# Kernel tuning notes

Measured on AMD Instinct MI355X. Metric: run time of the kernel, lower is better.

Reference implementation:

```python
import jax, jax.numpy as jnp
import numpy as np

N, E, H, NF, EF = 50000, 400000, 128, 10, 10


def setup_inputs() -> dict:
    key = jax.random.key(0)
    ks = iter(jax.random.split(key, 24))
    rn = lambda shape, s=0.1: jax.random.normal(next(ks), shape, jnp.float32) * s
    z = lambda shape: jnp.zeros(shape, jnp.float32)
    o = lambda shape: jnp.ones(shape, jnp.float32)
    return {
        "x": jax.random.normal(next(ks), (N, NF), jnp.float32),
        "edge_index": jax.random.randint(next(ks), (2, E), 0, N, jnp.int32),
        "edge_attr": jax.random.normal(next(ks), (E, EF), jnp.float32),
        "ne_w": rn((NF, H)), "ne_b": z(H), "ne_g": o(H), "ne_beta": z(H),
        "ee_w": rn((EF, H)), "ee_b": z(H), "ee_g": o(H), "ee_beta": z(H),
        "gate_w": rn((3 * H, H)), "gate_b": z(H),
        "gatA_w": rn((2, H, H)), "gatA_asrc": rn((2, 8, 16)), "gatA_adst": rn((2, 8, 16)), "gatA_bias": z((2, H)),
        "gatB_w": rn((H, H)), "gatB_asrc": rn((1, H)), "gatB_adst": rn((1, H)), "gatB_bias": z(H),
        "ln_g": o((3, H)), "ln_b": z((3, H)),
        "c1_w": rn((2 * H, H)), "c1_b": z(H), "cl1_g": o(H), "cl1_b": z(H),
        "c2_w": rn((H, H // 2)), "c2_b": z(H // 2), "cl2_g": o(H // 2), "cl2_b": z(H // 2),
        "c3_w": rn((H // 2, 2)), "c3_b": z(2),
    }


def _ln(x, g, b):
    m = x.mean(-1, keepdims=True)
    v = ((x - m) ** 2).mean(-1, keepdims=True)
    return (x - m) / jnp.sqrt(v + 1e-5) * g + b


def _gat(h, src, dst, n, w, asrc, adst, bias, concat):
    # PyG GATConv: lin (no bias), per-edge leaky_relu score, segment softmax over dst, scatter-add
    heads, dout = asrc.shape
    xp = (h @ w).reshape(n, heads, dout)             # [N, heads, dout]
    a_s = (xp * asrc).sum(-1)                        # [N, heads]
    a_d = (xp * adst).sum(-1)
    e = jax.nn.leaky_relu(a_s[src] + a_d[dst], 0.2)  # [E2, heads]
    m = jax.ops.segment_max(e, dst, num_segments=n)
    ex = jnp.exp(e - m[dst])
    s = jax.ops.segment_sum(ex, dst, num_segments=n)
    alpha = ex / s[dst]                               # [E2, heads]
    out = jax.ops.segment_sum(xp[src] * alpha[..., None], dst, num_segments=n)  # [N, heads, dout]
    out = out.reshape(n, heads * dout) if concat else out.mean(1)
    return out + bias


def reference(x, edge_index, edge_attr, ne_w, ne_b, ne_g, ne_beta, ee_w, ee_b, ee_g, ee_beta,
              gate_w, gate_b, gatA_w, gatA_asrc, gatA_adst, gatA_bias, gatB_w, gatB_asrc,
              gatB_adst, gatB_bias, ln_g, ln_b, c1_w, c1_b, cl1_g, cl1_b, c2_w, c2_b,
              cl2_g, cl2_b, c3_w, c3_b):
    n = x.shape[0]
    row, col = edge_index[0], edge_index[1]
    loops = jnp.arange(n, dtype=edge_index.dtype)     # GATConv add_self_loops=True
    src_sl = jnp.concatenate([row, loops])
    dst_sl = jnp.concatenate([col, loops])

    h = jax.nn.relu(_ln(x @ ne_w + ne_b, ne_g, ne_beta))      # node encoder (dropout=eval)
    for l in range(2):
        h = _gat(h, src_sl, dst_sl, n, gatA_w[l], gatA_asrc[l], gatA_adst[l], gatA_bias[l], True)
        h = jax.nn.relu(_ln(h, ln_g[l], ln_b[l]))
    h = _gat(h, src_sl, dst_sl, n, gatB_w, gatB_asrc, gatB_adst, gatB_bias, False)
    h = jax.nn.relu(_ln(h, ln_g[2], ln_b[2]))

    s = h[row]
    d = h[col]
    e = jax.nn.relu(_ln(edge_attr @ ee_w + ee_b, ee_g, ee_beta))  # edge encoder
    gate = jax.nn.sigmoid(jnp.concatenate([s, d, e], axis=1) @ gate_w + gate_b)
    s = s + gate * e
    d = d + gate * e

    zc = jax.nn.relu(_ln(jnp.concatenate([s, d], axis=1) @ c1_w + c1_b, cl1_g, cl1_b))
    zc = jax.nn.relu(_ln(zc @ c2_w + c2_b, cl2_g, cl2_b))
    return zc @ c3_w + c3_b                                   # [E, num_classes]
```

## Files before the change

### kernel.cpp

```cpp
#include <hip/hip_runtime.h>
#include <hip/hip_bf16.h>

#define H 128
#define NFEAT 10
#define EFEAT 10
#define XPS 144

typedef __attribute__((ext_vector_type(8))) short bf16x8;
typedef __attribute__((ext_vector_type(4))) float f32x4;
typedef __attribute__((ext_vector_type(16))) float f32x16;
typedef __attribute__((ext_vector_type(4))) unsigned u32x4;
typedef __attribute__((ext_vector_type(2))) unsigned u32x2;

__device__ __forceinline__ float bflo(unsigned v) { return __uint_as_float(v << 16); }
__device__ __forceinline__ float bfhi(unsigned v) { return __uint_as_float(v & 0xffff0000u); }
__device__ __forceinline__ unsigned bfpack(float a, float b) {
    __hip_bfloat16 h0 = __float2bfloat16(a), h1 = __float2bfloat16(b);
    return (unsigned)(*(unsigned short*)&h0) | ((unsigned)(*(unsigned short*)&h1) << 16);
}
__device__ __forceinline__ bf16x8 cast8(u32x4 v) { return __builtin_bit_cast(bf16x8, v); }

__device__ __forceinline__ bf16x8 frag_from_pack(const unsigned* w, int b2) {
    u32x4 t;
    t.x = w[b2 * 4 + 0];
    t.y = w[b2 * 4 + 1];
    t.z = w[b2 * 4 + 2];
    t.w = w[b2 * 4 + 3];
    return cast8(t);
}

__device__ __forceinline__ void ld8(bf16x8* dst, const __hip_bfloat16* base, int slot0, int l) {
#pragma unroll
    for (int i = 0; i < 8; i++)
        dst[i] = *(const bf16x8*)(base + ((size_t)(slot0 + i) * 64 + l) * 8);
}
__device__ __forceinline__ void ld4(bf16x8* dst, const __hip_bfloat16* base, int slot0, int l) {
#pragma unroll
    for (int i = 0; i < 4; i++)
        dst[i] = *(const bf16x8*)(base + ((size_t)(slot0 + i) * 64 + l) * 8);
}
__device__ __forceinline__ void mma8(f32x16* acc, const bf16x8* wb, bf16x8 bb0, bf16x8 bb1) {
#pragma unroll
    for (int mt = 0; mt < 4; mt++)
        acc[mt] = __builtin_amdgcn_mfma_f32_32x32x16_bf16(wb[mt], bb0, acc[mt], 0, 0, 0);
#pragma unroll
    for (int mt = 0; mt < 4; mt++)
        acc[mt] = __builtin_amdgcn_mfma_f32_32x32x16_bf16(wb[4 + mt], bb1, acc[mt], 0, 0, 0);
}
__device__ __forceinline__ void mma4x2(f32x16* acc, const bf16x8* wb, bf16x8 bb0, bf16x8 bb1) {
#pragma unroll
    for (int mt = 0; mt < 2; mt++)
        acc[mt] = __builtin_amdgcn_mfma_f32_32x32x16_bf16(wb[mt], bb0, acc[mt], 0, 0, 0);
#pragma unroll
    for (int mt = 0; mt < 2; mt++)
        acc[mt] = __builtin_amdgcn_mfma_f32_32x32x16_bf16(wb[2 + mt], bb1, acc[mt], 0, 0, 0);
}

template<int NT>
__device__ __forceinline__ void bias_ln_relu_pack(f32x16* acc, const float* __restrict__ bias,
        const float* __restrict__ g, const float* __restrict__ beta,
        int hh, float invn, unsigned (*pk)[8]) {
    float sm = 0.f;
#pragma unroll
    for (int m = 0; m < NT; m++) {
#pragma unroll
        for (int P = 0; P < 4; P++) {
            f32x4 bv = *(const f32x4*)&bias[m * 32 + P * 8 + hh * 4];
#pragma unroll
            for (int u = 0; u < 4; u++) {
                float v = acc[m][P * 4 + u] + bv[u];
                acc[m][P * 4 + u] = v;
                sm += v;
            }
        }
    }
    sm += __shfl_xor(sm, 32, 64);
    float mean = sm * invn;
    float q = 0.f;
#pragma unroll
    for (int m = 0; m < NT; m++) {
#pragma unroll
        for (int r = 0; r < 16; r++) { float d = acc[m][r] - mean; q += d * d; }
    }
    q += __shfl_xor(q, 32, 64);
    float rstd = rsqrtf(q * invn + 1e-5f);
#pragma unroll
    for (int m = 0; m < NT; m++) {
#pragma unroll
        for (int P = 0; P < 4; P++) {
            f32x4 gv = *(const f32x4*)&g[m * 32 + P * 8 + hh * 4];
            f32x4 bz = *(const f32x4*)&beta[m * 32 + P * 8 + hh * 4];
#pragma unroll
            for (int u = 0; u < 4; u++) {
                float y = fmaxf((acc[m][P * 4 + u] - mean) * rstd * gv[u] + bz[u], 0.f);
                acc[m][P * 4 + u] = y;
            }
        }
    }
#pragma unroll
    for (int m = 0; m < NT; m++) {
#pragma unroll
        for (int p = 0; p < 8; p++) pk[m][p] = bfpack(acc[m][2 * p], acc[m][2 * p + 1]);
    }
}

__global__ __launch_bounds__(256) void k_degree(const int* __restrict__ col,
                                                int* __restrict__ deg, int E, int N) {
    int i = blockIdx.x * blockDim.x + threadIdx.x;
    int E2 = E + N;
    if (i < E2) {
        int d = (i < E) ? col[i] : (i - E);
        atomicAdd(&deg[d], 1);
    }
}

__global__ __launch_bounds__(1024) void k_scan(const int* __restrict__ deg,
                                               int* __restrict__ offs,
                                               int* __restrict__ cursor, int N) {
    __shared__ int ps[1024];
    int t = threadIdx.x;
    int chunk = (N + 1023) / 1024;
    int begin = t * chunk;
    int end = begin + chunk; if (end > N) end = N;
    int s = 0;
    for (int i = begin; i < end; i++) s += deg[i];
    if (begin >= N) s = 0;
    ps[t] = s;
    __syncthreads();
    for (int off = 1; off < 1024; off <<= 1) {
        int v = (t >= off) ? ps[t - off] : 0;
        __syncthreads();
        ps[t] += v;
        __syncthreads();
    }
    int run = (t == 0) ? 0 : ps[t - 1];
    if (begin < N) {
        for (int i = begin; i < end; i++) {
            offs[i] = run;
            cursor[i] = run;
            run += deg[i];
        }
    }
    if (t == 1023) offs[N] = ps[1023];
}

__global__ __launch_bounds__(256) void k_scatter(const int* __restrict__ rowp,
                                                 const int* __restrict__ colp,
                                                 int* __restrict__ cursor,
                                                 int* __restrict__ srcs, int E, int N) {
    int i = blockIdx.x * blockDim.x + threadIdx.x;
    if (i < E + N) {
        int s, d;
        if (i < E) { s = rowp[i]; d = colp[i]; }
        else       { s = i - E;  d = i - E; }
        int pos = atomicAdd(&cursor[d], 1);
        srcs[pos] = s;
    }
}

__global__ __launch_bounds__(256) void k_node_enc(const float* __restrict__ x,
                                                  const float* __restrict__ wm,
                                                  const float* __restrict__ b,
                                                  const float* __restrict__ g,
                                                  const float* __restrict__ beta,
                                                  __hip_bfloat16* __restrict__ h, int N) {
    int t = threadIdx.x;
    int w = t >> 6, l = t & 63;
    int n = blockIdx.x * 4 + w;
    if (n >= N) return;
    float xs[NFEAT];
#pragma unroll
    for (int k = 0; k < NFEAT; k++) xs[k] = x[(size_t)n * NFEAT + k];
    float a0 = b[2 * l], a1 = b[2 * l + 1];
#pragma unroll
    for (int k = 0; k < NFEAT; k++) {
        float2 wv = *(const float2*)&wm[k * H + 2 * l];
        a0 += xs[k] * wv.x;
        a1 += xs[k] * wv.y;
    }
    float p = a0 + a1;
#pragma unroll
    for (int s = 1; s < 64; s <<= 1) p += __shfl_xor(p, s, 64);
    float mean = p * (1.0f / H);
    float d0 = a0 - mean, d1 = a1 - mean;
    float q = d0 * d0 + d1 * d1;
#pragma unroll
    for (int s = 1; s < 64; s <<= 1) q += __shfl_xor(q, s, 64);
    float rstd = rsqrtf(q * (1.0f / H) + 1e-5f);
    float y0 = fmaxf(d0 * rstd * g[2 * l] + beta[2 * l], 0.0f);
    float y1 = fmaxf(d1 * rstd * g[2 * l + 1] + beta[2 * l + 1], 0.0f);
    *(unsigned*)&h[(size_t)n * H + 2 * l] = bfpack(y0, y1);
}

__global__ __launch_bounds__(256, 2) void k_gat_xp_mfma(
        const __hip_bfloat16* __restrict__ h_bf,
        const __hip_bfloat16* __restrict__ wT,
        const float* __restrict__ asrc,
        const float* __restrict__ adst,
        __hip_bfloat16* __restrict__ xp_bf,
        float* __restrict__ a_d,
        int heads, int N) {
    __shared__ __hip_bfloat16 Ws[128 * 136];
    __shared__ __hip_bfloat16 As[64 * 136];
    int t = threadIdx.x;
    int n0 = blockIdx.x * 64;

#pragma unroll
    for (int it = 0; it < 2; it++) {
        int idx = it * 256 + t;
        int row = idx >> 2, seg = idx & 3;
        const uint4* src = (const uint4*)(wT + row * 128 + seg * 32);
        uint4 v0 = src[0], v1 = src[1], v2 = src[2], v3 = src[3];
        uint4* dst = (uint4*)&Ws[row * 136 + seg * 32];
        dst[0] = v0; dst[1] = v1; dst[2] = v2; dst[3] = v3;
    }
    {
        int row = t >> 2, seg = t & 3;
        int n = n0 + row; if (n >= N) n = N - 1;
        const uint4* src = (const uint4*)(h_bf + (size_t)n * 128 + seg * 32);
        uint4 v0 = src[0], v1 = src[1], v2 = src[2], v3 = src[3];
        uint4* dst = (uint4*)&As[row * 136 + seg * 32];
        dst[0] = v0; dst[1] = v1; dst[2] = v2; dst[3] = v3;
    }
    __syncthreads();

    int w = t >> 6, l = t & 63, ln15 = l & 15, quad = l >> 4, q8 = quad * 8;
    f32x4 acc[8] = {};
#pragma unroll
    for (int k = 0; k < 128; k += 32) {
        bf16x8 af = *(const bf16x8*)&As[(w * 16 + ln15) * 136 + k + q8];
#pragma unroll
        for (int i = 0; i < 8; i++) {
            bf16x8 bfr = *(const bf16x8*)&Ws[(i * 16 + ln15) * 136 + k + q8];
            acc[i] = __builtin_amdgcn_mfma_f32_16x16x32_bf16(af, bfr, acc[i], 0, 0, 0);
        }
    }

    if (heads == 8) {
#pragma unroll
        for (int i = 0; i < 8; i++) {
            float av = asrc[i * 16 + ln15], dvv = adst[i * 16 + ln15];
            float ps[4], pd[4];
#pragma unroll
            for (int r = 0; r < 4; r++) { ps[r] = acc[i][r] * av; pd[r] = acc[i][r] * dvv; }
#pragma unroll
            for (int s = 1; s < 16; s <<= 1) {
#pragma unroll
                for (int r = 0; r < 4; r++) {
                    ps[r] += __shfl_xor(ps[r], s, 64);
                    pd[r] += __shfl_xor(pd[r], s, 64);
                }
            }
            if (ln15 == 0) {
#pragma unroll
                for (int r = 0; r < 4; r++) {
                    int n = n0 + w * 16 + quad * 4 + r;
                    if (n < N) {
                        *(float*)&xp_bf[(size_t)n * XPS + 128 + 2 * i] = ps[r];
                        a_d[(size_t)n * 8 + i] = pd[r];
                    }
                }
            }
        }
    } else {
        float ps[4] = {0, 0, 0, 0}, pd[4] = {0, 0, 0, 0};
#pragma unroll
        for (int i = 0; i < 8; i++) {
            float av = asrc[i * 16 + ln15], dvv = adst[i * 16 + ln15];
#pragma unroll
            for (int r = 0; r < 4; r++) { ps[r] += acc[i][r] * av; pd[r] += acc[i][r] * dvv; }
        }
#pragma unroll
        for (int s = 1; s < 16; s <<= 1) {
#pragma unroll
            for (int r = 0; r < 4; r++) {
                ps[r] += __shfl_xor(ps[r], s, 64);
                pd[r] += __shfl_xor(pd[r], s, 64);
            }
        }
        if (ln15 == 0) {
#pragma unroll
            for (int r = 0; r < 4; r++) {
                int n = n0 + w * 16 + quad * 4 + r;
                if (n < N) {
                    *(float*)&xp_bf[(size_t)n * XPS + 128] = ps[r];
                    a_d[n] = pd[r];
                }
            }
        }
    }

#pragma unroll
    for (int i = 0; i < 8; i++) {
#pragma unroll
        for (int r = 0; r < 4; r++) {
            int n = n0 + w * 16 + quad * 4 + r;
            if (n < N) xp_bf[(size_t)n * XPS + i * 16 + ln15] = __float2bfloat16(acc[i][r]);
        }
    }
}

__global__ __launch_bounds__(256) void k_gat_agg(const __hip_bfloat16* __restrict__ xp,
                                                 const float* __restrict__ a_d,
                                                 const int* __restrict__ offs,
                                                 const int* __restrict__ srcs,
                                                 const float* __restrict__ bias,
                                                 const float* __restrict__ g,
                                                 const float* __restrict__ b,
                                                 __hip_bfloat16* __restrict__ hout,
                                                 int heads, int N) {
    int t = threadIdx.x;
    int w = t >> 6, l = t & 63;
    int n = blockIdx.x * 4 + w;
    if (n >= N) return;
    int head = (heads == 8) ? (l >> 3) : 0;
    float adv = a_d[(size_t)n * heads + head];
    int s0 = offs[n], s1 = offs[n + 1];
    float acc0 = 0.0f, acc1 = 0.0f, den = 0.0f;
    int j = s0;
    for (; j + 8 <= s1; j += 8) {
        int s_[8];
#pragma unroll
        for (int u = 0; u < 8; u++) s_[u] = srcs[j + u];
        float e_[8]; unsigned v_[8];
#pragma unroll
        for (int u = 0; u < 8; u++) {
            const __hip_bfloat16* xr = xp + (size_t)s_[u] * XPS;
            e_[u] = ((const float*)xr)[64 + head];
            v_[u] = *(const unsigned*)&xr[2 * l];
        }
#pragma unroll
        for (int u = 0; u < 8; u++) {
            float e = e_[u] + adv;
            e = (e >= 0.0f) ? e : 0.2f * e;
            float ex = __expf(e);
            den += ex;
            acc0 += ex * bflo(v_[u]);
            acc1 += ex * bfhi(v_[u]);
        }
    }
    for (; j + 4 <= s1; j += 4) {
        int s_[4];
#pragma unroll
        for (int u = 0; u < 4; u++) s_[u] = srcs[j + u];
        float e_[4]; unsigned v_[4];
#pragma unroll
        for (int u = 0; u < 4; u++) {
            const __hip_bfloat16* xr = xp + (size_t)s_[u] * XPS;
            e_[u] = ((const float*)xr)[64 + head];
            v_[u] = *(const unsigned*)&xr[2 * l];
        }
#pragma unroll
        for (int u = 0; u < 4; u++) {
            float e = e_[u] + adv;
            e = (e >= 0.0f) ? e : 0.2f * e;
            float ex = __expf(e);
            den += ex;
            acc0 += ex * bflo(v_[u]);
            acc1 += ex * bfhi(v_[u]);
        }
    }
    for (; j < s1; j++) {
        int s = srcs[j];
        const __hip_bfloat16* xr = xp + (size_t)s * XPS;
        float e = ((const float*)xr)[64 + head] + adv;
        e = (e >= 0.0f) ? e : 0.2f * e;
        float ex = __expf(e);
        den += ex;
        unsigned v = *(const unsigned*)&xr[2 * l];
        acc0 += ex * bflo(v);
        acc1 += ex * bfhi(v);
    }
    float inv = 1.0f / den;
    float v0 = acc0 * inv + bias[2 * l];
    float v1 = acc1 * inv + bias[2 * l + 1];
    float p = v0 + v1;
#pragma unroll
    for (int s = 1; s < 64; s <<= 1) p += __shfl_xor(p, s, 64);
    float mean = p * (1.0f / H);
    float d0 = v0 - mean, d1 = v1 - mean;
    float q = d0 * d0 + d1 * d1;
#pragma unroll
    for (int s = 1; s < 64; s <<= 1) q += __shfl_xor(q, s, 64);
    float rstd = rsqrtf(q * (1.0f / H) + 1e-5f);
    float y0 = fmaxf(d0 * rstd * g[2 * l] + b[2 * l], 0.0f);
    float y1 = fmaxf(d1 * rstd * g[2 * l + 1] + b[2 * l + 1], 0.0f);
    *(unsigned*)&hout[(size_t)n * H + 2 * l] = bfpack(y0, y1);
}

__global__ __launch_bounds__(256) void k_wprep(const float* __restrict__ gate_w,
                                               const float* __restrict__ c1_w,
                                               const float* __restrict__ c2_w,
                                               const float* __restrict__ gatA_w,
                                               const float* __restrict__ gatB_w,
                                               const float* __restrict__ ee_w,
                                               __hip_bfloat16* __restrict__ gate_sw,
                                               __hip_bfloat16* __restrict__ c1_sw,
                                               __hip_bfloat16* __restrict__ c2_sw,
                                               __hip_bfloat16* __restrict__ wT3,
                                               __hip_bfloat16* __restrict__ ee_sw) {
    int i = blockIdx.x * blockDim.x + threadIdx.x;
    if (i < 49152) {
        int j = i & 7, l = (i >> 3) & 63, s = i >> 9;
        int m = s & 3, ks = s >> 2;
        int hh = l >> 5;
        int k;
        if (ks < 8) k = 256 + ks * 16 + 4 * hh + (j & 3) + 8 * (j >> 2);
        else        k = (ks - 8) * 16 + hh * 8 + j;
        int n = m * 32 + (l & 31);
        gate_sw[i] = __float2bfloat16(gate_w[k * 128 + n]);
    } else if (i < 81920) {
        int mm = i - 49152;
        int j = mm & 7, l = (mm >> 3) & 63, s = mm >> 9;
        int m = s & 3, ks = s >> 2;
        int k = ks * 16 + 4 * (l >> 5) + (j & 3) + 8 * (j >> 2);
        int n = m * 32 + (l & 31);
        c1_sw[mm] = __float2bfloat16(c1_w[k * 128 + n]);
    } else if (i < 90112) {
        int mm = i - 81920;
        int j = mm & 7, l = (mm >> 3) & 63, s = mm >> 9;
        int m = s & 1, ks = s >> 1;
        int k = ks * 16 + 4 * (l >> 5) + (j & 3) + 8 * (j >> 2);
        int n = m * 32 + (l & 31);
        c2_sw[mm] = __float2bfloat16(c2_w[k * 64 + n]);
    } else if (i < 139264) {
        int m = i - 90112;
        int mat = m / 16384, r = m % 16384;
        int n = r / 128, k = r % 128;
        const float* src = (mat < 2) ? (gatA_w + (size_t)mat * 16384) : gatB_w;
        wT3[m] = __float2bfloat16(src[k * 128 + n]);
    } else if (i < 141312) {
        int mm = i - 139264;
        int j = mm & 7, l = (mm >> 3) & 63, s = mm >> 9;
        int k = (l >> 5) * 8 + j;
        int n = s * 32 + (l & 31);
        ee_sw[mm] = (k < EFEAT) ? __float2bfloat16(ee_w[k * 128 + n]) : __float2bfloat16(0.0f);
    }
}

__global__ __launch_bounds__(256, 2) void k_edge_cls_mfma32(
        const __hip_bfloat16* __restrict__ h_bf,
        const int* __restrict__ rowp, const int* __restrict__ colp,
        const float* __restrict__ eattr,
        const __hip_bfloat16* __restrict__ ee_fa, const float* __restrict__ ee_b,
        const float* __restrict__ ee_g, const float* __restrict__ ee_beta,
        const __hip_bfloat16* __restrict__ gate_fa, const float* __restrict__ gate_b,
        const __hip_bfloat16* __restrict__ c1_fa, const float* __restrict__ c1_b,
        const float* __restrict__ cl1_g, const float* __restrict__ cl1_b,
        const __hip_bfloat16* __restrict__ c2_fa, const float* __restrict__ c2_b,
        const float* __restrict__ cl2_g, const float* __restrict__ cl2_b,
        const float* __restrict__ c3_w, const float* __restrict__ c3_b,
        float* __restrict__ out, int E) {
    int t = threadIdx.x;
    int w = t >> 6, l = t & 63;
    int hh = l >> 5, e32 = l & 31;
    int eIdx = blockIdx.x * 128 + w * 32 + e32;
    int eF = (eIdx < E) ? eIdx : (E - 1);
    int ri = rowp[eF], ci = colp[eF];
    const unsigned short* rS = (const unsigned short*)h_bf + (size_t)ri * H;
    const unsigned short* rD = (const unsigned short*)h_bf + (size_t)ci * H;

    bf16x8 wbA[8], wbB[8];

    unsigned efw[4][8];
    {
        const char* eb = (const char*)(eattr + (size_t)eF * EFEAT);
        float2 p0 = *(const float2*)(eb + (hh << 5));
        float2 p1 = *(const float2*)(eb + 8);
        float2 p2 = *(const float2*)(eb + 16);
        float2 p3 = *(const float2*)(eb + 24);
        bf16x8 eef[4];
        ld4(eef, ee_fa, 0, l);
        if (hh) { p1.x = p1.y = 0.f; p2.x = p2.y = 0.f; p3.x = p3.y = 0.f; }
        u32x4 bwv;
        bwv.x = bfpack(p0.x, p0.y);
        bwv.y = bfpack(p1.x, p1.y);
        bwv.z = bfpack(p2.x, p2.y);
        bwv.w = bfpack(p3.x, p3.y);
        bf16x8 bb = cast8(bwv);
        f32x16 acc[4] = {};
#pragma unroll
        for (int m = 0; m < 4; m++)
            acc[m] = __builtin_amdgcn_mfma_f32_32x32x16_bf16(eef[m], bb, acc[m], 0, 0, 0);
        ld8(wbA, gate_fa, 0, l);
        bias_ln_relu_pack<4>(acc, ee_b, ee_g, ee_beta, hh, 1.f / 128.f, efw);
    }

    f32x16 acc1[4] = {};
    {
        bf16x8 sfr[8], dfr[8];
        ld8(wbB, gate_fa, 8, l);
        mma8(acc1, wbA, frag_from_pack(efw[0], 0), frag_from_pack(efw[0], 1));
        ld8(wbA, gate_fa, 16, l);
        mma8(acc1, wbB, frag_from_pack(efw[1], 0), frag_from_pack(efw[1], 1));
#pragma unroll
        for (int i = 0; i < 8; i++) sfr[i] = *(const bf16x8*)(rS + i * 16 + hh * 8);
        ld8(wbB, gate_fa, 24, l);
        mma8(acc1, wbA, frag_from_pack(efw[2], 0), frag_from_pack(efw[2], 1));
        ld8(wbA, gate_fa, 32, l);
        mma8(acc1, wbB, frag_from_pack(efw[3], 0), frag_from_pack(efw[3], 1));
#pragma unroll
        for (int i = 0; i < 8; i++) dfr[i] = *(const bf16x8*)(rD + i * 16 + hh * 8);
        ld8(wbB, gate_fa, 40, l);
        mma8(acc1, wbA, sfr[0], sfr[1]);
        ld8(wbA, gate_fa, 48, l);
        mma8(acc1, wbB, sfr[2], sfr[3]);
        ld8(wbB, gate_fa, 56, l);
        mma8(acc1, wbA, sfr[4], sfr[5]);
        ld8(wbA, gate_fa, 64, l);
        mma8(acc1, wbB, sfr[6], sfr[7]);
        ld8(wbB, gate_fa, 72, l);
        mma8(acc1, wbA, dfr[0], dfr[1]);
        ld8(wbA, gate_fa, 80, l);
        mma8(acc1, wbB, dfr[2], dfr[3]);
        ld8(wbB, gate_fa, 88, l);
        mma8(acc1, wbA, dfr[4], dfr[5]);
        ld8(wbA, c1_fa, 0, l);
        mma8(acc1, wbB, dfr[6], dfr[7]);
    }

    unsigned sw[4][8], dw[4][8];
    {
#pragma unroll
        for (int m = 0; m < 4; m++) {
#pragma unroll
            for (int P = 0; P < 4; P++) {
                int f0 = m * 32 + P * 8 + hh * 4;
                f32x4 gb = *(const f32x4*)&gate_b[f0];
                u32x2 sv = *(const u32x2*)(rS + f0);
                u32x2 dv = *(const u32x2*)(rD + f0);
#pragma unroll
                for (int u2 = 0; u2 < 2; u2++) {
                    int p = P * 2 + u2;
                    unsigned svw = u2 ? sv.y : sv.x;
                    unsigned dvw = u2 ? dv.y : dv.x;
                    float g0 = acc1[m][2 * p] + gb[2 * u2];
                    float g1 = acc1[m][2 * p + 1] + gb[2 * u2 + 1];
                    g0 = 1.f / (1.f + __expf(-g0));
                    g1 = 1.f / (1.f + __expf(-g1));
                    float e0 = bflo(efw[m][p]), e1 = bfhi(efw[m][p]);
                    sw[m][p] = bfpack(bflo(svw) + g0 * e0, bfhi(svw) + g1 * e1);
                    dw[m][p] = bfpack(bflo(dvw) + g0 * e0, bfhi(dvw) + g1 * e1);
                }
            }
        }
    }

    unsigned z1w[4][8];
    bf16x8 wcA[4], wcB[4];
    {
        f32x16 acc2[4] = {};
        ld8(wbB, c1_fa, 8, l);
        mma8(acc2, wbA, frag_from_pack(sw[0], 0), frag_from_pack(sw[0], 1));
        ld8(wbA, c1_fa, 16, l);
        mma8(acc2, wbB, frag_from_pack(sw[1], 0), frag_from_pack(sw[1], 1));
        ld8(wbB, c1_fa, 24, l);
        mma8(acc2, wbA, frag_from_pack(sw[2], 0), frag_from_pack(sw[2], 1));
        ld8(wbA, c1_fa, 32, l);
        mma8(acc2, wbB, frag_from_pack(sw[3], 0), frag_from_pack(sw[3], 1));
        ld8(wbB, c1_fa, 40, l);
        mma8(acc2, wbA, frag_from_pack(dw[0], 0), frag_from_pack(dw[0], 1));
        ld8(wbA, c1_fa, 48, l);
        mma8(acc2, wbB, frag_from_pack(dw[1], 0), frag_from_pack(dw[1], 1));
        ld8(wbB, c1_fa, 56, l);
        mma8(acc2, wbA, frag_from_pack(dw[2], 0), frag_from_pack(dw[2], 1));
        ld4(wcA, c2_fa, 0, l);
        mma8(acc2, wbB, frag_from_pack(dw[3], 0), frag_from_pack(dw[3], 1));
        bias_ln_relu_pack<4>(acc2, c1_b, cl1_g, cl1_b, hh, 1.f / 128.f, z1w);
    }

    {
        f32x16 acc3[2] = {};
        ld4(wcB, c2_fa, 4, l);
        mma4x2(acc3, wcA, frag_from_pack(z1w[0], 0), frag_from_pack(z1w[0], 1));
        ld4(wcA, c2_fa, 8, l);
        mma4x2(acc3, wcB, frag_from_pack(z1w[1], 0), frag_from_pack(z1w[1], 1));
        ld4(wcB, c2_fa, 12, l);
        mma4x2(acc3, wcA, frag_from_pack(z1w[2], 0), frag_from_pack(z1w[2], 1));
        mma4x2(acc3, wcB, frag_from_pack(z1w[3], 0), frag_from_pack(z1w[3], 1));
        float sm = 0.f;
#pragma unroll
        for (int m = 0; m < 2; m++) {
#pragma unroll
            for (int P = 0; P < 4; P++) {
                f32x4 bv = *(const f32x4*)&c2_b[m * 32 + P * 8 + hh * 4];
#pragma unroll
                for (int u = 0; u < 4; u++) {
                    float v = acc3[m][P * 4 + u] + bv[u];
                    acc3[m][P * 4 + u] = v;
                    sm += v;
                }
            }
        }
        sm += __shfl_xor(sm, 32, 64);
        float mean = sm * (1.f / 64.f);
        float q = 0.f;
#pragma unroll
        for (int m = 0; m < 2; m++) {
#pragma unroll
            for (int r = 0; r < 16; r++) { float d = acc3[m][r] - mean; q += d * d; }
        }
        q += __shfl_xor(q, 32, 64);
        float rstd = rsqrtf(q * (1.f / 64.f) + 1e-5f);
        float s0 = 0.f, s1 = 0.f;
#pragma unroll
        for (int m = 0; m < 2; m++) {
#pragma unroll
            for (int P = 0; P < 4; P++) {
                int f0 = m * 32 + P * 8 + hh * 4;
                f32x4 gv = *(const f32x4*)&cl2_g[f0];
                f32x4 bz = *(const f32x4*)&cl2_b[f0];
                f32x4 wA = *(const f32x4*)&c3_w[f0 * 2];
                f32x4 wB = *(const f32x4*)&c3_w[f0 * 2 + 4];
#pragma unroll
                for (int u = 0; u < 4; u++) {
                    float y = fmaxf((acc3[m][P * 4 + u] - mean) * rstd * gv[u] + bz[u], 0.f);
                    float wc0 = (u < 2) ? wA[2 * u] : wB[2 * u - 4];
                    float wc1 = (u < 2) ? wA[2 * u + 1] : wB[2 * u - 3];
                    s0 += y * wc0;
                    s1 += y * wc1;
                }
            }
        }
        s0 += __shfl_xor(s0, 32, 64);
        s1 += __shfl_xor(s1, 32, 64);
        if (hh == 0 && eIdx < E) {
            float2 o; o.x = s0 + c3_b[0]; o.y = s1 + c3_b[1];
            *(float2*)&out[(size_t)eIdx * 2] = o;
        }
    }
}

extern "C" void kernel_launch(void* const* d_in, const int* in_sizes, int n_in,
                              void* d_out, int out_size, void* d_ws, size_t ws_size,
                              hipStream_t stream) {
    const float* x        = (const float*)d_in[0];
    const int*   eidx     = (const int*)d_in[1];
    const float* eattr    = (const float*)d_in[2];
    const float* ne_w     = (const float*)d_in[3];
    const float* ne_b     = (const float*)d_in[4];
    const float* ne_g     = (const float*)d_in[5];
    const float* ne_beta  = (const float*)d_in[6];
    const float* ee_w     = (const float*)d_in[7];
    const float* ee_b     = (const float*)d_in[8];
    const float* ee_g     = (const float*)d_in[9];
    const float* ee_beta  = (const float*)d_in[10];
    const float* gate_w   = (const float*)d_in[11];
    const float* gate_b   = (const float*)d_in[12];
    const float* gatA_w   = (const float*)d_in[13];
    const float* gatA_as  = (const float*)d_in[14];
    const float* gatA_ad  = (const float*)d_in[15];
    const float* gatA_bias= (const float*)d_in[16];
    const float* gatB_w   = (const float*)d_in[17];
    const float* gatB_as  = (const float*)d_in[18];
    const float* gatB_ad  = (const float*)d_in[19];
    const float* gatB_bias= (const float*)d_in[20];
    const float* ln_g     = (const float*)d_in[21];
    const float* ln_b     = (const float*)d_in[22];
    const float* c1_w     = (const float*)d_in[23];
    const float* c1_b     = (const float*)d_in[24];
    const float* cl1_g    = (const float*)d_in[25];
    const float* cl1_b    = (const float*)d_in[26];
    const float* c2_w     = (const float*)d_in[27];
    const float* c2_b     = (const float*)d_in[28];
    const float* cl2_g    = (const float*)d_in[29];
    const float* cl2_b    = (const float*)d_in[30];
    const float* c3_w     = (const float*)d_in[31];
    const float* c3_b     = (const float*)d_in[32];

    const int N = in_sizes[0] / NFEAT;
    const int E = in_sizes[1] / 2;
    const int E2 = E + N;
    const int* rowp = eidx;
    const int* colp = eidx + E;

    char* ws = (char*)d_ws;
    size_t off = 0;
    auto alloc = [&](size_t bytes) -> void* {
        void* p = ws + off;
        off = (off + bytes + 255) & ~(size_t)255;
        return p;
    };
    int*   deg    = (int*)alloc((size_t)N * 4);
    int*   cursor = (int*)alloc((size_t)N * 4);
    int*   offs   = (int*)alloc((size_t)(N + 1) * 4);
    int*   srcs   = (int*)alloc((size_t)E2 * 4);
    float* a_d    = (float*)alloc((size_t)N * 8 * 4);
    __hip_bfloat16* h_bfA  = (__hip_bfloat16*)alloc((size_t)N * H * 2);
    __hip_bfloat16* h_bfB  = (__hip_bfloat16*)alloc((size_t)N * H * 2);
    __hip_bfloat16* xp_bf  = (__hip_bfloat16*)alloc((size_t)N * XPS * 2);
    __hip_bfloat16* gate_sw= (__hip_bfloat16*)alloc((size_t)49152 * 2);
    __hip_bfloat16* c1_sw  = (__hip_bfloat16*)alloc((size_t)32768 * 2);
    __hip_bfloat16* c2_sw  = (__hip_bfloat16*)alloc((size_t)8192 * 2);
    __hip_bfloat16* wT3    = (__hip_bfloat16*)alloc((size_t)3 * 128 * 128 * 2);
    __hip_bfloat16* ee_sw  = (__hip_bfloat16*)alloc((size_t)4096 * 2);
    (void)ws_size;

    k_wprep<<<(141312 + 255) / 256, 256, 0, stream>>>(gate_w, c1_w, c2_w, gatA_w, gatB_w, ee_w,
                                                      gate_sw, c1_sw, c2_sw, wT3, ee_sw);

    hipMemsetAsync(deg, 0, (size_t)N * 4, stream);
    k_degree<<<(E2 + 255) / 256, 256, 0, stream>>>(colp, deg, E, N);
    k_scan<<<1, 1024, 0, stream>>>(deg, offs, cursor, N);
    k_scatter<<<(E2 + 255) / 256, 256, 0, stream>>>(rowp, colp, cursor, srcs, E, N);

    int ngrid = (N + 3) / 4;
    k_node_enc<<<ngrid, 256, 0, stream>>>(x, ne_w, ne_b, ne_g, ne_beta, h_bfA, N);

    int xpgrid = (N + 63) / 64;
    __hip_bfloat16* hin = h_bfA;
    __hip_bfloat16* hout = h_bfB;
    for (int l = 0; l < 2; l++) {
        k_gat_xp_mfma<<<xpgrid, 256, 0, stream>>>(hin, wT3 + (size_t)l * 16384,
                                                  gatA_as + l * H, gatA_ad + l * H,
                                                  xp_bf, a_d, 8, N);
        k_gat_agg<<<ngrid, 256, 0, stream>>>(xp_bf, a_d, offs, srcs,
                                             gatA_bias + l * H, ln_g + l * H, ln_b + l * H,
                                             hout, 8, N);
        __hip_bfloat16* tmp = hin; hin = hout; hout = tmp;
    }
    k_gat_xp_mfma<<<xpgrid, 256, 0, stream>>>(hin, wT3 + (size_t)2 * 16384,
                                              gatB_as, gatB_ad,
                                              xp_bf, a_d, 1, N);
    k_gat_agg<<<ngrid, 256, 0, stream>>>(xp_bf, a_d, offs, srcs,
                                         gatB_bias, ln_g + 2 * H, ln_b + 2 * H,
                                         hout, 1, N);

    k_edge_cls_mfma32<<<(E + 127) / 128, 256, 0, stream>>>(
        hout, rowp, colp, eattr,
        ee_sw, ee_b, ee_g, ee_beta,
        gate_sw, gate_b,
        c1_sw, c1_b, cl1_g, cl1_b,
        c2_sw, c2_b, cl2_g, cl2_b,
        c3_w, c3_b,
        (float*)d_out, E);
}
```

Before: 661.1 us.

## Merge front-end kernels into one launch and parallelize the degree scan

Weight preparation, degree counting and node encoding, which are independent, now run as block ranges of a single kernel launch instead of three separate launches. The single-block serial-chunk prefix scan over node degrees is replaced by a three-pass multi-block scan: per-block sums, a scan of block sums, then per-block local scans. The aim is to cut launch overhead and the long single-workgroup scan latency, at the cost of two extra small launches and a branchy fused kernel.

```diff
diff --git a/kernel.cpp b/kernel.cpp
--- a/kernel.cpp
+++ b/kernel.cpp
@@ -104,44 +104,154 @@
     }
 }
 
-__global__ __launch_bounds__(256) void k_degree(const int* __restrict__ col,
-                                                int* __restrict__ deg, int E, int N) {
-    int i = blockIdx.x * blockDim.x + threadIdx.x;
-    int E2 = E + N;
-    if (i < E2) {
-        int d = (i < E) ? col[i] : (i - E);
-        atomicAdd(&deg[d], 1);
-    }
-}
-
-__global__ __launch_bounds__(1024) void k_scan(const int* __restrict__ deg,
+__global__ __launch_bounds__(256) void k_front(
+        const float* __restrict__ gate_w, const float* __restrict__ c1_w,
+        const float* __restrict__ c2_w, const float* __restrict__ gatA_w,
+        const float* __restrict__ gatB_w, const float* __restrict__ ee_w,
+        __hip_bfloat16* __restrict__ gate_sw, __hip_bfloat16* __restrict__ c1_sw,
+        __hip_bfloat16* __restrict__ c2_sw, __hip_bfloat16* __restrict__ wT3,
+        __hip_bfloat16* __restrict__ ee_sw,
+        const int* __restrict__ colp, int* __restrict__ deg,
+        const float* __restrict__ x, const float* __restrict__ ne_w,
+        const float* __restrict__ ne_b, const float* __restrict__ ne_g,
+        const float* __restrict__ ne_beta, __hip_bfloat16* __restrict__ h,
+        int E, int N, int nbWprep, int nbDeg) {
+    int blk = blockIdx.x;
+    if (blk < nbWprep) {
+        int i = blk * 256 + threadIdx.x;
+        if (i < 49152) {
+            int j = i & 7, l = (i >> 3) & 63, s = i >> 9;
+            int m = s & 3, ks = s >> 2;
+            int hh = l >> 5;
+            int k;
+            if (ks < 8) k = 256 + ks * 16 + 4 * hh + (j & 3) + 8 * (j >> 2);
+            else        k = (ks - 8) * 16 + hh * 8 + j;
+            int n = m * 32 + (l & 31);
+            gate_sw[i] = __float2bfloat16(gate_w[k * 128 + n]);
+        } else if (i < 81920) {
+            int mm = i - 49152;
+            int j = mm & 7, l = (mm >> 3) & 63, s = mm >> 9;
+            int m = s & 3, ks = s >> 2;
+            int k = ks * 16 + 4 * (l >> 5) + (j & 3) + 8 * (j >> 2);
+            int n = m * 32 + (l & 31);
+            c1_sw[mm] = __float2bfloat16(c1_w[k * 128 + n]);
+        } else if (i < 90112) {
+            int mm = i - 81920;
+            int j = mm & 7, l = (mm >> 3) & 63, s = mm >> 9;
+            int m = s & 1, ks = s >> 1;
+            int k = ks * 16 + 4 * (l >> 5) + (j & 3) + 8 * (j >> 2);
+            int n = m * 32 + (l & 31);
+            c2_sw[mm] = __float2bfloat16(c2_w[k * 64 + n]);
+        } else if (i < 139264) {
+            int m = i - 90112;
+            int mat = m / 16384, r = m % 16384;
+            int n = r / 128, k = r % 128;
+            const float* src = (mat < 2) ? (gatA_w + (size_t)mat * 16384) : gatB_w;
+            wT3[m] = __float2bfloat16(src[k * 128 + n]);
+        } else if (i < 141312) {
+            int mm = i - 139264;
+            int j = mm & 7, l = (mm >> 3) & 63, s = mm >> 9;
+            int k = (l >> 5) * 8 + j;
+            int n = s * 32 + (l & 31);
+            ee_sw[mm] = (k < EFEAT) ? __float2bfloat16(ee_w[k * 128 + n])
+                                    : __float2bfloat16(0.0f);
+        }
+        return;
+    }
+    blk -= nbWprep;
+    if (blk < nbDeg) {
+        int i = blk * 256 + threadIdx.x;
+        int E2 = E + N;
+        if (i < E2) {
+            int d = (i < E) ? colp[i] : (i - E);
+            atomicAdd(&deg[d], 1);
+        }
+        return;
+    }
+    blk -= nbDeg;
+    {
+        int t = threadIdx.x;
+        int w = t >> 6, l = t & 63;
+        int n = blk * 4 + w;
+        if (n >= N) return;
+        float xs[NFEAT];
+#pragma unroll
+        for (int k = 0; k < NFEAT; k++) xs[k] = x[(size_t)n * NFEAT + k];
+        float a0 = ne_b[2 * l], a1 = ne_b[2 * l + 1];
+#pragma unroll
+        for (int k = 0; k < NFEAT; k++) {
+            float2 wv = *(const float2*)&ne_w[k * H + 2 * l];
+            a0 += xs[k] * wv.x;
+            a1 += xs[k] * wv.y;
+        }
+        float p = a0 + a1;
+#pragma unroll
+        for (int s = 1; s < 64; s <<= 1) p += __shfl_xor(p, s, 64);
+        float mean = p * (1.0f / H);
+        float d0 = a0 - mean, d1 = a1 - mean;
+        float q = d0 * d0 + d1 * d1;
+#pragma unroll
+        for (int s = 1; s < 64; s <<= 1) q += __shfl_xor(q, s, 64);
+        float rstd = rsqrtf(q * (1.0f / H) + 1e-5f);
+        float y0 = fmaxf(d0 * rstd * ne_g[2 * l] + ne_beta[2 * l], 0.0f);
+        float y1 = fmaxf(d1 * rstd * ne_g[2 * l + 1] + ne_beta[2 * l + 1], 0.0f);
+        *(unsigned*)&h[(size_t)n * H + 2 * l] = bfpack(y0, y1);
+    }
+}
+
+__global__ __launch_bounds__(256) void k_scanA(const int* __restrict__ deg,
+                                               int* __restrict__ bsum, int N) {
+    __shared__ int s[256];
+    int t = threadIdx.x;
+    int i = blockIdx.x * 256 + t;
+    s[t] = (i < N) ? deg[i] : 0;
+    __syncthreads();
+    for (int off = 128; off > 0; off >>= 1) {
+        if (t < off) s[t] += s[t + off];
+        __syncthreads();
+    }
+    if (t == 0) bsum[blockIdx.x] = s[0];
+}
+
+__global__ __launch_bounds__(1024) void k_scanB(int* __restrict__ bsum, int NB) {
+    __shared__ int s[1024];
+    int t = threadIdx.x;
+    int v = (t < NB) ? bsum[t] : 0;
+    s[t] = v;
+    __syncthreads();
+    for (int off = 1; off < 1024; off <<= 1) {
+        int u = (t >= off) ? s[t - off] : 0;
+        __syncthreads();
+        s[t] += u;
+        __syncthreads();
+    }
+    if (t < NB) bsum[t] = s[t] - v;
+}
+
+__global__ __launch_bounds__(256) void k_scanC(const int* __restrict__ deg,
+                                               const int* __restrict__ bbase,
                                                int* __restrict__ offs,
                                                int* __restrict__ cursor, int N) {
-    __shared__ int ps[1024];
+    __shared__ int s[256];
     int t = threadIdx.x;
-    int chunk = (N + 1023) / 1024;
-    int begin = t * chunk;
-    int end = begin + chunk; if (end > N) end = N;
-    int s = 0;
-    for (int i = begin; i < end; i++) s += deg[i];
-    if (begin >= N) s = 0;
-    ps[t] = s;
+    int i = blockIdx.x * 256 + t;
+    int v = (i < N) ? deg[i] : 0;
+    s[t] = v;
     __syncthreads();
-    for (int off = 1; off < 1024; off <<= 1) {
-        int v = (t >= off) ? ps[t - off] : 0;
+    for (int off = 1; off < 256; off <<= 1) {
+        int u = (t >= off) ? s[t - off] : 0;
         __syncthreads();
-        ps[t] += v;
+        s[t] += u;
         __syncthreads();
     }
-    int run = (t == 0) ? 0 : ps[t - 1];
-    if (begin < N) {
-        for (int i = begin; i < end; i++) {
-            offs[i] = run;
-            cursor[i] = run;
-            run += deg[i];
-        }
-    }
-    if (t == 1023) offs[N] = ps[1023];
+    int incl = s[t];
+    int base = bbase[blockIdx.x];
+    if (i < N) {
+        int e = base + incl - v;
+        offs[i] = e;
+        cursor[i] = e;
+        if (i == N - 1) offs[N] = base + incl;
+    }
 }
 
 __global__ __launch_bounds__(256) void k_scatter(const int* __restrict__ rowp,
@@ -156,40 +266,6 @@
         int pos = atomicAdd(&cursor[d], 1);
         srcs[pos] = s;
     }
-}
-
-__global__ __launch_bounds__(256) void k_node_enc(const float* __restrict__ x,
-                                                  const float* __restrict__ wm,
-                                                  const float* __restrict__ b,
-                                                  const float* __restrict__ g,
-                                                  const float* __restrict__ beta,
-                                                  __hip_bfloat16* __restrict__ h, int N) {
-    int t = threadIdx.x;
-    int w = t >> 6, l = t & 63;
-    int n = blockIdx.x * 4 + w;
-    if (n >= N) return;
-    float xs[NFEAT];
-#pragma unroll
-    for (int k = 0; k < NFEAT; k++) xs[k] = x[(size_t)n * NFEAT + k];
-    float a0 = b[2 * l], a1 = b[2 * l + 1];
-#pragma unroll
-    for (int k = 0; k < NFEAT; k++) {
-        float2 wv = *(const float2*)&wm[k * H + 2 * l];
-        a0 += xs[k] * wv.x;
-        a1 += xs[k] * wv.y;
-    }
-    float p = a0 + a1;
-#pragma unroll
-    for (int s = 1; s < 64; s <<= 1) p += __shfl_xor(p, s, 64);
-    float mean = p * (1.0f / H);
-    float d0 = a0 - mean, d1 = a1 - mean;
-    float q = d0 * d0 + d1 * d1;
-#pragma unroll
-    for (int s = 1; s < 64; s <<= 1) q += __shfl_xor(q, s, 64);
-    float rstd = rsqrtf(q * (1.0f / H) + 1e-5f);
-    float y0 = fmaxf(d0 * rstd * g[2 * l] + beta[2 * l], 0.0f);
-    float y1 = fmaxf(d1 * rstd * g[2 * l + 1] + beta[2 * l + 1], 0.0f);
-    *(unsigned*)&h[(size_t)n * H + 2 * l] = bfpack(y0, y1);
 }
 
 __global__ __launch_bounds__(256, 2) void k_gat_xp_mfma(
@@ -386,56 +462,6 @@
     float y0 = fmaxf(d0 * rstd * g[2 * l] + b[2 * l], 0.0f);
     float y1 = fmaxf(d1 * rstd * g[2 * l + 1] + b[2 * l + 1], 0.0f);
     *(unsigned*)&hout[(size_t)n * H + 2 * l] = bfpack(y0, y1);
-}
-
-__global__ __launch_bounds__(256) void k_wprep(const float* __restrict__ gate_w,
-                                               const float* __restrict__ c1_w,
-                                               const float* __restrict__ c2_w,
-                                               const float* __restrict__ gatA_w,
-                                               const float* __restrict__ gatB_w,
-                                               const float* __restrict__ ee_w,
-                                               __hip_bfloat16* __restrict__ gate_sw,
-                                               __hip_bfloat16* __restrict__ c1_sw,
-                                               __hip_bfloat16* __restrict__ c2_sw,
-                                               __hip_bfloat16* __restrict__ wT3,
-                                               __hip_bfloat16* __restrict__ ee_sw) {
-    int i = blockIdx.x * blockDim.x + threadIdx.x;
-    if (i < 49152) {
-        int j = i & 7, l = (i >> 3) & 63, s = i >> 9;
-        int m = s & 3, ks = s >> 2;
-        int hh = l >> 5;
-        int k;
-        if (ks < 8) k = 256 + ks * 16 + 4 * hh + (j & 3) + 8 * (j >> 2);
-        else        k = (ks - 8) * 16 + hh * 8 + j;
-        int n = m * 32 + (l & 31);
-        gate_sw[i] = __float2bfloat16(gate_w[k * 128 + n]);
-    } else if (i < 81920) {
-        int mm = i - 49152;
-        int j = mm & 7, l = (mm >> 3) & 63, s = mm >> 9;
-        int m = s & 3, ks = s >> 2;
-        int k = ks * 16 + 4 * (l >> 5) + (j & 3) + 8 * (j >> 2);
-        int n = m * 32 + (l & 31);
-        c1_sw[mm] = __float2bfloat16(c1_w[k * 128 + n]);
-    } else if (i < 90112) {
-        int mm = i - 81920;
-        int j = mm & 7, l = (mm >> 3) & 63, s = mm >> 9;
-        int m = s & 1, ks = s >> 1;
-        int k = ks * 16 + 4 * (l >> 5) + (j & 3) + 8 * (j >> 2);
-        int n = m * 32 + (l & 31);
-        c2_sw[mm] = __float2bfloat16(c2_w[k * 64 + n]);
-    } else if (i < 139264) {
-        int m = i - 90112;
-        int mat = m / 16384, r = m % 16384;
-        int n = r / 128, k = r % 128;
-        const float* src = (mat < 2) ? (gatA_w + (size_t)mat * 16384) : gatB_w;
-        wT3[m] = __float2bfloat16(src[k * 128 + n]);
-    } else if (i < 141312) {
-        int mm = i - 139264;
-        int j = mm & 7, l = (mm >> 3) & 63, s = mm >> 9;
-        int k = (l >> 5) * 8 + j;
-        int n = s * 32 + (l & 31);
-        ee_sw[mm] = (k < EFEAT) ? __float2bfloat16(ee_w[k * 128 + n]) : __float2bfloat16(0.0f);
-    }
 }
 
 __global__ __launch_bounds__(256, 2) void k_edge_cls_mfma32(
@@ -685,6 +711,7 @@
     int*   cursor = (int*)alloc((size_t)N * 4);
     int*   offs   = (int*)alloc((size_t)(N + 1) * 4);
     int*   srcs   = (int*)alloc((size_t)E2 * 4);
+    int*   bsum   = (int*)alloc((size_t)1024 * 4);
     float* a_d    = (float*)alloc((size_t)N * 8 * 4);
     __hip_bfloat16* h_bfA  = (__hip_bfloat16*)alloc((size_t)N * H * 2);
     __hip_bfloat16* h_bfB  = (__hip_bfloat16*)alloc((size_t)N * H * 2);
@@ -696,17 +723,24 @@
     __hip_bfloat16* ee_sw  = (__hip_bfloat16*)alloc((size_t)4096 * 2);
     (void)ws_size;
 
-    k_wprep<<<(141312 + 255) / 256, 256, 0, stream>>>(gate_w, c1_w, c2_w, gatA_w, gatB_w, ee_w,
-                                                      gate_sw, c1_sw, c2_sw, wT3, ee_sw);
-
+    const int nbWprep = (141312 + 255) / 256;
+    const int nbDeg   = (E2 + 255) / 256;
+    const int nbEnc   = (N + 3) / 4;
     hipMemsetAsync(deg, 0, (size_t)N * 4, stream);
-    k_degree<<<(E2 + 255) / 256, 256, 0, stream>>>(colp, deg, E, N);
-    k_scan<<<1, 1024, 0, stream>>>(deg, offs, cursor, N);
+    k_front<<<nbWprep + nbDeg + nbEnc, 256, 0, stream>>>(
+        gate_w, c1_w, c2_w, gatA_w, gatB_w, ee_w,
+        gate_sw, c1_sw, c2_sw, wT3, ee_sw,
+        colp, deg,
+        x, ne_w, ne_b, ne_g, ne_beta, h_bfA,
+        E, N, nbWprep, nbDeg);
+
+    const int NB = (N + 255) / 256;
+    k_scanA<<<NB, 256, 0, stream>>>(deg, bsum, N);
+    k_scanB<<<1, 1024, 0, stream>>>(bsum, NB);
+    k_scanC<<<NB, 256, 0, stream>>>(deg, bsum, offs, cursor, N);
     k_scatter<<<(E2 + 255) / 256, 256, 0, stream>>>(rowp, colp, cursor, srcs, E, N);
 
     int ngrid = (N + 3) / 4;
-    k_node_enc<<<ngrid, 256, 0, stream>>>(x, ne_w, ne_b, ne_g, ne_beta, h_bfA, N);
-
     int xpgrid = (N + 63) / 64;
     __hip_bfloat16* hin = h_bfA;
     __hip_bfloat16* hout = h_bfB;
```

After: 557.3 us (median of 2 runs). 1.19x faster.
